# Performance work log

Measured on AMD Instinct MI355X. Metric: run time of the kernel, lower is better.

The kernel has to match this reference:

```python
import jax, jax.numpy as jnp
import numpy as np

# n-gram trie hyperparameters (match torch module invariants exactly)
V = 8192          # vocabulary size
N = 3             # n-gram order (trigram)
SHIFT = 0         # no sos/eos shift
C2, C3 = 32, 8    # children per unigram node / per bigram node
U = V + SHIFT + 1
B2 = U * C2                  # bigram node count
B3 = B2 * C3                 # trigram node count
X = U + B2 + 1               # pointers length (level 1..N-1 nodes + dummy)
G = B3 - 1
K = X + G - U                # ids length == B2 + B3
L = 2 * X + G                # logs length
S_MAX = max(C2, C3)          # static max branching factor (torch computes it dynamically)
BATCH = 128


def _build_trie():
    rng = np.random.RandomState(0)
    u = np.arange(U, dtype=np.int32)
    i = np.arange(B2, dtype=np.int32)
    # pointers[node] = first_child_index(node) - node; dummy last entry closes counts
    ptr_uni = (U + u.astype(np.int64) * C2 - u).astype(np.int32)
    ptr_bi = (B2 + i.astype(np.int64) * (C3 - 1)).astype(np.int32)
    pointers = np.concatenate([ptr_uni, ptr_bi, np.array([B3], dtype=np.int32)])
    # child token ids: distinct per parent (strides 251, 977 coprime-ish, C*stride < V)
    ids_bi = ((u[:, None].astype(np.int64) * 17 + np.arange(C2)[None, :] * 251) % V).reshape(-1).astype(np.int32)
    ids_tri = ((i[:, None].astype(np.int64) * 13 + np.arange(C3)[None, :] * 977) % V).reshape(-1).astype(np.int32)
    ids = np.concatenate([ids_bi, ids_tri])
    n_nodes = U + B2 + B3    # == X + G
    logs = np.concatenate([
        -rng.uniform(1.0, 10.0, n_nodes),   # conditional log-probs per node
        -rng.uniform(0.1, 2.0, X),          # backoff weights for nodes 0..X-1
    ]).astype(np.float32)
    assert ids.size == K and logs.size == L
    return jnp.asarray(pointers), jnp.asarray(ids), jnp.asarray(logs)


def setup_inputs() -> dict:
    key = jax.random.key(0)
    pointers, ids, logs = _build_trie()
    hist = jax.random.randint(key, (N - 1, BATCH), 0, V, dtype=jnp.int32)
    return {"hist": hist, "idx": N - 1, "pointers": pointers, "ids": ids, "logs": logs}


def _forward(hist, idx, pointers, ids, logs):
    B = hist.shape[1]
    M = B * V
    h = hist[:idx][-(N - 1):]                                 # (N-1, B), idx >= N-1
    vr = jnp.arange(V, dtype=hist.dtype)
    cur = jnp.broadcast_to(vr[None, None, :], (1, B, V))
    h = jnp.concatenate(
        [jnp.broadcast_to(h[:, :, None], (N - 1, B, V)), cur], 0
    ).reshape(N, M)                                           # (N, M) token grid

    srange = jnp.arange(S_MAX, dtype=jnp.int32)
    out = jnp.zeros(M, jnp.float32)
    running = jnp.ones(M, bool)
    children = tokens = h[0]
    for Nn in range(N - 1):
        n = N - Nn
        offsets = pointers[children]
        num_children = pointers[children + 1] - offsets + 1
        first_children = children + offsets
        step_mask = running
        for t in range(1, n):
            tokens = h[Nn + t]
            all_children = first_children[:, None] + srange[None, :]  # (M, S_MAX)
            matches = (
                (ids[jnp.clip(all_children, None, K + U - 1) - U] == tokens[:, None])
                & (srange[None, :] < num_children[:, None])
                & step_mask[:, None]
            )
            next_step = matches.any(1)
            if t == n - 1:
                logs_t = jnp.where(matches, logs[all_children], 0.0).sum(1)
                finite = jnp.isfinite(logs_t)
                out = jnp.where(finite, out + logs_t, out)
                next_step = next_step & finite
                running = running & ~next_step
                new_backoff = step_mask & ~next_step
                out = jnp.where(new_backoff, out + logs[X + G + children], out)
            else:
                children = jnp.where(matches, all_children, 0).sum(1)
                offsets = pointers[children]
                num_children = pointers[children + 1] - offsets + 1
                first_children = children + offsets
            step_mask = next_step
        children = tokens = h[Nn + 1]
    out = jnp.where(running, out + logs[tokens], out)
    return out.reshape(B, V)


def reference(hist, idx, pointers, ids, logs):
    return _forward(hist, idx, pointers, ids, logs)
```

## Files before the change

kernel.cpp:

```cpp
#include <hip/hip_runtime.h>

#define TV   8192
#define TU   8193
#define TB2  262176
#define TXP  270370
#define TG   2097407
#define TKU  2367776
#define CHUNKS 8
#define VCHUNK (TV / CHUNKS)

__global__ __launch_bounds__(256) void lookup_lm_kernel(
    const int* __restrict__ hist, const int* __restrict__ idxp,
    const int* __restrict__ pointers, const int* __restrict__ ids,
    const float* __restrict__ logs, float* __restrict__ out, int Bsz)
{
    __shared__ int   s_trig_id[8];
    __shared__ float s_trig_log[8];
    __shared__ int   s_big_id[32];
    __shared__ float s_big_log[32];
    __shared__ float s_base;
    __shared__ float s_bo1;
    __shared__ int   s_ctx;

    const int tid = threadIdx.x;
    const int b   = blockIdx.y;
    const int idx = idxp[0];
    const int h0  = hist[(idx - 2) * Bsz + b];
    const int h1  = hist[(idx - 1) * Bsz + b];

    if (tid == 0) s_ctx = -1;
    __syncthreads();

    if (tid < 32) {
        int off0 = pointers[h0];
        int nch0 = pointers[h0 + 1] - off0 + 1;
        int fc0  = h0 + off0;
        if (tid < nch0) {
            int node = fc0 + tid;
            int ci   = min(node, TKU) - TU;
            if (ids[ci] == h1) s_ctx = node;
        }
        int offb = pointers[h1];
        int nchb = pointers[h1 + 1] - offb + 1;
        int fcb  = h1 + offb;
        int bid = -1; float blog = 0.f;
        if (tid < nchb) {
            int node = fcb + tid;
            int ci   = min(node, TKU) - TU;
            bid  = ids[ci];
            blog = logs[node];
        }
        s_big_id[tid]  = bid;
        s_big_log[tid] = blog;
        if (tid == 0) s_bo1 = logs[TXP + TG + h1];
    }
    __syncthreads();

    const int ctx = s_ctx;
    if (tid < 8) {
        int tidv = -1; float tlog = 0.f;
        if (ctx >= 0) {
            int off1 = pointers[ctx];
            int nch1 = pointers[ctx + 1] - off1 + 1;
            int fc1  = ctx + off1;
            if (tid < nch1) {
                int node = fc1 + tid;
                int ci   = min(node, TKU) - TU;
                tidv = ids[ci];
                tlog = logs[node];
            }
            if (tid == 0) s_base = logs[TXP + TG + ctx];
        } else if (tid == 0) {
            s_base = 0.f;
        }
        s_trig_id[tid]  = tidv;
        s_trig_log[tid] = tlog;
    }
    __syncthreads();

    const float base = s_base;
    const float bo1  = s_bo1;
    const int vbase  = blockIdx.x * VCHUNK;
    float* orow = out + (size_t)b * TV;

    for (int i = tid; i < VCHUNK / 4; i += 256) {
        int v0 = vbase + i * 4;
        float4 lg = *reinterpret_cast<const float4*>(logs + v0);
        float lgv[4] = {lg.x, lg.y, lg.z, lg.w};
        float r[4];
        #pragma unroll
        for (int j = 0; j < 4; ++j) {
            int v = v0 + j;
            float tlog = 0.f; bool tri = false;
            #pragma unroll
            for (int s = 0; s < 8; ++s) {
                if (s_trig_id[s] == v) { tlog = s_trig_log[s]; tri = true; }
            }
            float blog = 0.f; bool bi = false;
            #pragma unroll
            for (int s = 0; s < 32; ++s) {
                if (s_big_id[s] == v) { blog = s_big_log[s]; bi = true; }
            }
            float fallback = base + (bi ? blog : (bo1 + lgv[j]));
            r[j] = tri ? tlog : fallback;
        }
        float4 res = make_float4(r[0], r[1], r[2], r[3]);
        *reinterpret_cast<float4*>(orow + v0) = res;
    }
}

extern "C" void kernel_launch(void* const* d_in, const int* in_sizes, int n_in,
                              void* d_out, int out_size, void* d_ws, size_t ws_size,
                              hipStream_t stream) {
    const int*   hist     = (const int*)d_in[0];
    const int*   idxp     = (const int*)d_in[1];
    const int*   pointers = (const int*)d_in[2];
    const int*   ids      = (const int*)d_in[3];
    const float* logs     = (const float*)d_in[4];
    float* out = (float*)d_out;

    const int B = in_sizes[0] / 2;
    dim3 grid(CHUNKS, B);
    lookup_lm_kernel<<<grid, 256, 0, stream>>>(hist, idxp, pointers, ids, logs, out, B);
}
```

Baseline: 10.37 us.

## Scatter trie overrides into shared table and parallelize pointer loads

Replaces the per-element linear scan over 8 trigram and 32 bigram children with a shared-memory override table. Children are scattered into the table once and each output element is resolved with a single lookup. The second-level pointer reads are prefetched in parallel by otherwise idle threads, and the logs/pointer loads are issued before the first barrier, which shortens the serial dependent-load chain. In exchange it adds extra barriers and relies on an infinity sentinel, which would be wrong if a real log value were +inf.

```diff
diff --git a/kernel.cpp b/kernel.cpp
--- a/kernel.cpp
+++ b/kernel.cpp
@@ -2,111 +2,112 @@
 
 #define TV   8192
 #define TU   8193
-#define TB2  262176
 #define TXP  270370
 #define TG   2097407
 #define TKU  2367776
 #define CHUNKS 8
 #define VCHUNK (TV / CHUNKS)
+#define SENT 0x7F800000u
 
 __global__ __launch_bounds__(256) void lookup_lm_kernel(
     const int* __restrict__ hist, const int* __restrict__ idxp,
     const int* __restrict__ pointers, const int* __restrict__ ids,
     const float* __restrict__ logs, float* __restrict__ out, int Bsz)
 {
-    __shared__ int   s_trig_id[8];
-    __shared__ float s_trig_log[8];
-    __shared__ int   s_big_id[32];
-    __shared__ float s_big_log[32];
+    __shared__ unsigned s_over[VCHUNK];
+    __shared__ int   s_ptr[33];
     __shared__ float s_base;
     __shared__ float s_bo1;
     __shared__ int   s_ctx;
 
-    const int tid = threadIdx.x;
-    const int b   = blockIdx.y;
-    const int idx = idxp[0];
-    const int h0  = hist[(idx - 2) * Bsz + b];
-    const int h1  = hist[(idx - 1) * Bsz + b];
+    const int tid   = threadIdx.x;
+    const int b     = blockIdx.y;
+    const int vbase = blockIdx.x * VCHUNK;
 
+    float4 lg4 = *reinterpret_cast<const float4*>(logs + vbase + tid * 4);
+    int h0  = hist[b];
+    int h1  = hist[Bsz + b];
+    int idx = idxp[0];
+    if (idx != 2) {
+        h0 = hist[(idx - 2) * Bsz + b];
+        h1 = hist[(idx - 1) * Bsz + b];
+    }
+
+    *reinterpret_cast<uint4*>(&s_over[tid * 4]) = make_uint4(SENT, SENT, SENT, SENT);
     if (tid == 0) s_ctx = -1;
+
+    const int p_h0  = pointers[h0];
+    const int p_h0n = pointers[h0 + 1];
+    const int p_h1  = pointers[h1];
+    const int p_h1n = pointers[h1 + 1];
+
+    const int fc0  = h0 + p_h0;
+    const int nch0 = p_h0n - p_h0 + 1;
+    const int fcb  = h1 + p_h1;
+    const int nchb = p_h1n - p_h1 + 1;
+
     __syncthreads();
 
+    int big_id = -1; float big_log = 0.f;
     if (tid < 32) {
-        int off0 = pointers[h0];
-        int nch0 = pointers[h0 + 1] - off0 + 1;
-        int fc0  = h0 + off0;
         if (tid < nch0) {
             int node = fc0 + tid;
-            int ci   = min(node, TKU) - TU;
-            if (ids[ci] == h1) s_ctx = node;
+            int cid  = ids[min(node, TKU) - TU];
+            if (cid == h1) s_ctx = node;
         }
-        int offb = pointers[h1];
-        int nchb = pointers[h1 + 1] - offb + 1;
-        int fcb  = h1 + offb;
-        int bid = -1; float blog = 0.f;
-        if (tid < nchb) {
-            int node = fcb + tid;
-            int ci   = min(node, TKU) - TU;
-            bid  = ids[ci];
-            blog = logs[node];
+    } else if (tid < 64) {
+        int s = tid - 32;
+        if (s < nchb) {
+            int node = fcb + s;
+            big_id  = ids[min(node, TKU) - TU];
+            big_log = logs[node];
         }
-        s_big_id[tid]  = bid;
-        s_big_log[tid] = blog;
-        if (tid == 0) s_bo1 = logs[TXP + TG + h1];
+    } else if (tid < 97) {
+        s_ptr[tid - 64] = pointers[fc0 + (tid - 64)];
+    } else if (tid == 97) {
+        s_bo1 = logs[TXP + TG + h1];
     }
     __syncthreads();
 
     const int ctx = s_ctx;
-    if (tid < 8) {
-        int tidv = -1; float tlog = 0.f;
-        if (ctx >= 0) {
-            int off1 = pointers[ctx];
-            int nch1 = pointers[ctx + 1] - off1 + 1;
-            int fc1  = ctx + off1;
-            if (tid < nch1) {
-                int node = fc1 + tid;
-                int ci   = min(node, TKU) - TU;
-                tidv = ids[ci];
-                tlog = logs[node];
+    int tri_id = -1; float tri_log = 0.f;
+    if (ctx >= 0) {
+        if (tid < 8) {
+            int ci   = ctx - fc0;
+            int offc = s_ptr[ci];
+            int nchc = s_ptr[ci + 1] - offc + 1;
+            if (tid < nchc) {
+                int node = ctx + offc + tid;
+                tri_id  = ids[min(node, TKU) - TU];
+                tri_log = logs[node];
             }
-            if (tid == 0) s_base = logs[TXP + TG + ctx];
-        } else if (tid == 0) {
-            s_base = 0.f;
+        } else if (tid == 8) {
+            s_base = logs[TXP + TG + ctx];
         }
-        s_trig_id[tid]  = tidv;
-        s_trig_log[tid] = tlog;
+    } else if (tid == 8) {
+        s_base = 0.f;
     }
     __syncthreads();
 
     const float base = s_base;
-    const float bo1  = s_bo1;
-    const int vbase  = blockIdx.x * VCHUNK;
-    float* orow = out + (size_t)b * TV;
 
-    for (int i = tid; i < VCHUNK / 4; i += 256) {
-        int v0 = vbase + i * 4;
-        float4 lg = *reinterpret_cast<const float4*>(logs + v0);
-        float lgv[4] = {lg.x, lg.y, lg.z, lg.w};
-        float r[4];
-        #pragma unroll
-        for (int j = 0; j < 4; ++j) {
-            int v = v0 + j;
-            float tlog = 0.f; bool tri = false;
-            #pragma unroll
-            for (int s = 0; s < 8; ++s) {
-                if (s_trig_id[s] == v) { tlog = s_trig_log[s]; tri = true; }
-            }
-            float blog = 0.f; bool bi = false;
-            #pragma unroll
-            for (int s = 0; s < 32; ++s) {
-                if (s_big_id[s] == v) { blog = s_big_log[s]; bi = true; }
-            }
-            float fallback = base + (bi ? blog : (bo1 + lgv[j]));
-            r[j] = tri ? tlog : fallback;
-        }
-        float4 res = make_float4(r[0], r[1], r[2], r[3]);
-        *reinterpret_cast<float4*>(orow + v0) = res;
+    if (big_id >= vbase && big_id < vbase + VCHUNK) {
+        s_over[big_id - vbase] = __float_as_uint(base + big_log);
     }
+    __syncthreads();
+    if (tri_id >= vbase && tri_id < vbase + VCHUNK) {
+        s_over[tri_id - vbase] = __float_as_uint(tri_log);
+    }
+    __syncthreads();
+
+    const float fb = base + s_bo1;
+    uint4 ov = *reinterpret_cast<const uint4*>(&s_over[tid * 4]);
+    float4 res;
+    res.x = (ov.x == SENT) ? fb + lg4.x : __uint_as_float(ov.x);
+    res.y = (ov.y == SENT) ? fb + lg4.y : __uint_as_float(ov.y);
+    res.z = (ov.z == SENT) ? fb + lg4.z : __uint_as_float(ov.z);
+    res.w = (ov.w == SENT) ? fb + lg4.w : __uint_as_float(ov.w);
+    *reinterpret_cast<float4*>(out + (size_t)b * TV + vbase + tid * 4) = res;
 }
 
 extern "C" void kernel_launch(void* const* d_in, const int* in_sizes, int n_in,
```

Measured after the change: 10.06 us, median of 2. 1.03x faster.
